# Performance work log

Measured on AMD Instinct MI355X. Metric: run time of the kernel, lower is better.

Reference implementation:

```python
import jax, jax.numpy as jnp
import numpy as np

B, N, D, H, S = 4, 32768, 256, 8, 64
DH = D // H  # 32


def setup_inputs() -> dict:
    key = jax.random.key(0)
    ks = jax.random.split(key, 8)
    s = 0.02
    return {
        "x": jax.random.normal(ks[0], (B, N, D), jnp.float32),
        "W_fx": jax.random.normal(ks[1], (D, D), jnp.float32) * s,
        "b_fx": jnp.zeros((D,), jnp.float32),
        "W_x": jax.random.normal(ks[2], (D, D), jnp.float32) * s,
        "b_x": jnp.zeros((D,), jnp.float32),
        "W_slice": jax.random.normal(ks[3], (DH, S), jnp.float32) * s,
        "b_slice": jnp.zeros((S,), jnp.float32),
        "temperature": jnp.full((1, H, 1, 1), 0.5, jnp.float32),
        "W_qkv": jax.random.normal(ks[4], (DH, 3 * DH), jnp.float32) * s,  # qkv_bias=False
        "W_out": jax.random.normal(ks[5], (D, D), jnp.float32) * s,
        "b_out": jnp.zeros((D,), jnp.float32),
    }


def reference(x, W_fx, b_fx, W_x, b_x, W_slice, b_slice, temperature, W_qkv, W_out, b_out):
    b, n, d = x.shape
    h, dh = H, d // H
    scale = dh ** -0.5
    # per-head projections: [b, h, n, dh]
    fx_mid = (x @ W_fx + b_fx).reshape(b, n, h, dh).transpose(0, 2, 1, 3)
    x_mid = (x @ W_x + b_x).reshape(b, n, h, dh).transpose(0, 2, 1, 3)
    # soft slice assignment: softmax over slices [b, h, n, s]
    logits = (x_mid @ W_slice + b_slice) / temperature
    slice_weights = jax.nn.softmax(logits, axis=-1)
    slice_norm = slice_weights.sum(axis=2)  # [b, h, s]
    # weighted pooling of points into slice tokens [b, h, s, dh]
    slice_token = jnp.einsum('bhnc,bhns->bhsc', fx_mid, slice_weights)
    slice_token = slice_token / (slice_norm[..., None] + 1e-5)
    # tiny attention among slice tokens
    q, k, v = jnp.split(slice_token @ W_qkv, 3, axis=-1)
    dots = jnp.einsum('bhsc,bhtc->bhst', q, k) * scale
    attn = jax.nn.softmax(dots, axis=-1)
    out_slice_token = attn @ v  # [b, h, s, dh]
    # scatter back to points [b, h, n, dh]
    out_x = jnp.einsum('bhsc,bhns->bhnc', out_slice_token, slice_weights)
    out_x = out_x.transpose(0, 2, 1, 3).reshape(b, n, d)
    return out_x @ W_out + b_out
```

## Files before the change

kernel.cpp:

```cpp
#include <hip/hip_runtime.h>
#include <math.h>

#define TS_N 32768
#define TS_M 131072

typedef short bf16x8 __attribute__((ext_vector_type(8)));
typedef float f32x4  __attribute__((ext_vector_type(4)));
typedef unsigned short us4 __attribute__((ext_vector_type(4)));
typedef unsigned short us8 __attribute__((ext_vector_type(8)));

static __device__ __forceinline__ unsigned short f2bf(float f) {
    unsigned u = __float_as_uint(f);
    u = u + 0x7FFF + ((u >> 16) & 1);
    return (unsigned short)(u >> 16);
}
static __device__ __forceinline__ float bf2f(unsigned short b) {
    return __uint_as_float(((unsigned)b) << 16);
}

__global__ __launch_bounds__(256) void k0_split(
    const float* __restrict__ src, unsigned short* __restrict__ h,
    unsigned short* __restrict__ l, int n4)
{
    for (int i = blockIdx.x * 256 + threadIdx.x; i < n4; i += gridDim.x * 256) {
        float4 v = ((const float4*)src)[i];
        us4 vh, vl;
        float c[4] = {v.x, v.y, v.z, v.w};
#pragma unroll
        for (int j = 0; j < 4; ++j) {
            unsigned short hh = f2bf(c[j]);
            vh[j] = hh;
            vl[j] = f2bf(c[j] - bf2f(hh));
        }
        ((us4*)h)[i] = vh;
        ((us4*)l)[i] = vl;
    }
}

__global__ __launch_bounds__(256) void k0_wt(
    const float* __restrict__ Wfx, const float* __restrict__ Wx,
    unsigned short* __restrict__ Wth, unsigned short* __restrict__ Wtl)
{
    const int n = blockIdx.x;
    const int wsel = blockIdx.y;
    const int k = threadIdx.x;
    const float v = (wsel ? Wx : Wfx)[k * 256 + n];
    const unsigned short hh = f2bf(v);
    const int idx = (wsel * 256 + n) * 256 + k;
    Wth[idx] = hh;
    Wtl[idx] = f2bf(v - bf2f(hh));
}

__global__ __launch_bounds__(256) void gemm_hl(
    const unsigned short* __restrict__ Ah, const unsigned short* __restrict__ Al,
    const unsigned short* __restrict__ Bth, const unsigned short* __restrict__ Btl,
    const float* __restrict__ bias, float* __restrict__ OUT,
    int K, long bsel)
{
    __shared__ unsigned short Alds[2][128 * 32];
    __shared__ unsigned short Blds[2][128 * 32];
    const int t = threadIdx.x;
    const int row0 = blockIdx.x * 128;
    const int n0 = blockIdx.y * 128;
    const long boff = (long)(row0 >> 15) * bsel;
    const unsigned short* Bhp = Bth + boff;
    const unsigned short* Blp = Btl + boff;

    const int w = t >> 6, l = t & 63;
    const int wm = w >> 1, wn = w & 1;
    const int lr = l & 15, lk = l >> 4;

    f32x4 acc[4][4];
#pragma unroll
    for (int i = 0; i < 4; ++i)
#pragma unroll
        for (int j = 0; j < 4; ++j) {
            acc[i][j][0] = 0.f; acc[i][j][1] = 0.f;
            acc[i][j][2] = 0.f; acc[i][j][3] = 0.f;
        }

    for (int kk = 0; kk < K; kk += 32) {
        bf16x8 stg[8];
#pragma unroll
        for (int g2i = 0; g2i < 2; ++g2i) {
            const int g2 = w + g2i * 4;
            const size_t ar = (size_t)(row0 + g2 * 16 + lr) * K + kk + lk * 8;
            const size_t br = (size_t)(n0 + g2 * 16 + lr) * K + kk + lk * 8;
            stg[g2i * 4 + 0] = *(const bf16x8*)&Ah[ar];
            stg[g2i * 4 + 1] = *(const bf16x8*)&Al[ar];
            stg[g2i * 4 + 2] = *(const bf16x8*)&Bhp[br];
            stg[g2i * 4 + 3] = *(const bf16x8*)&Blp[br];
        }
        __syncthreads();
#pragma unroll
        for (int g2i = 0; g2i < 2; ++g2i) {
            const int g2 = w + g2i * 4;
            const int lc = (g2 * 64 + l) * 8;
            *(bf16x8*)&Alds[0][lc] = stg[g2i * 4 + 0];
            *(bf16x8*)&Alds[1][lc] = stg[g2i * 4 + 1];
            *(bf16x8*)&Blds[0][lc] = stg[g2i * 4 + 2];
            *(bf16x8*)&Blds[1][lc] = stg[g2i * 4 + 3];
        }
        __syncthreads();

        bf16x8 ah[4], al[4], bh[4], bl[4];
#pragma unroll
        for (int g = 0; g < 4; ++g) {
            const int ac = (((wm * 4 + g) * 4 + lk) * 16 + lr) * 8;
            ah[g] = *(const bf16x8*)&Alds[0][ac];
            al[g] = *(const bf16x8*)&Alds[1][ac];
            const int bc = (((wn * 4 + g) * 4 + lk) * 16 + lr) * 8;
            bh[g] = *(const bf16x8*)&Blds[0][bc];
            bl[g] = *(const bf16x8*)&Blds[1][bc];
        }
#pragma unroll
        for (int m = 0; m < 4; ++m)
#pragma unroll
            for (int n = 0; n < 4; ++n) {
                acc[m][n] = __builtin_amdgcn_mfma_f32_16x16x32_bf16(ah[m], bh[n], acc[m][n], 0, 0, 0);
                acc[m][n] = __builtin_amdgcn_mfma_f32_16x16x32_bf16(ah[m], bl[n], acc[m][n], 0, 0, 0);
                acc[m][n] = __builtin_amdgcn_mfma_f32_16x16x32_bf16(al[m], bh[n], acc[m][n], 0, 0, 0);
            }
    }

    float bv[4];
#pragma unroll
    for (int n = 0; n < 4; ++n) bv[n] = bias[n0 + wn * 64 + n * 16 + lr];
#pragma unroll
    for (int m = 0; m < 4; ++m)
#pragma unroll
        for (int n = 0; n < 4; ++n) {
            const int col = n0 + wn * 64 + n * 16 + lr;
#pragma unroll
            for (int r = 0; r < 4; ++r) {
                const int row = row0 + wm * 64 + m * 16 + lk * 4 + r;
                OUT[(size_t)row * 256 + col] = acc[m][n][r] + bv[n];
            }
        }
}

__global__ __launch_bounds__(256) void k1b_slice_softmax(
    const float* __restrict__ XM, const float* __restrict__ Wsl,
    const float* __restrict__ bsl, const float* __restrict__ temp,
    unsigned short* __restrict__ SWh, unsigned short* __restrict__ SWl)
{
    __shared__ float XMs[32][68];
    __shared__ float Ws[32][68];
    __shared__ float Ls[64][68];
    const int t  = threadIdx.x;
    const int r0 = blockIdx.x * 64;
    const int h  = blockIdx.y;

    {
        const int m = t >> 2, cq = (t & 3) * 8;
        float4 v0 = *(const float4*)&XM[(size_t)(r0 + m) * 256 + h * 32 + cq];
        float4 v1 = *(const float4*)&XM[(size_t)(r0 + m) * 256 + h * 32 + cq + 4];
        XMs[cq + 0][m] = v0.x; XMs[cq + 1][m] = v0.y; XMs[cq + 2][m] = v0.z; XMs[cq + 3][m] = v0.w;
        XMs[cq + 4][m] = v1.x; XMs[cq + 5][m] = v1.y; XMs[cq + 6][m] = v1.z; XMs[cq + 7][m] = v1.w;
        const int wk = t >> 3, wn = (t & 7) * 8;
        float4 u0 = *(const float4*)&Wsl[wk * 64 + wn];
        float4 u1 = *(const float4*)&Wsl[wk * 64 + wn + 4];
        *(float4*)&Ws[wk][wn]     = u0;
        *(float4*)&Ws[wk][wn + 4] = u1;
    }
    __syncthreads();

    const int tx = t & 15, ty = t >> 4;
    float acc[4][4];
#pragma unroll
    for (int i = 0; i < 4; ++i)
#pragma unroll
        for (int j = 0; j < 4; ++j) acc[i][j] = 0.f;
#pragma unroll
    for (int c = 0; c < 32; ++c) {
        float4 av = *(const float4*)&XMs[c][ty * 4];
        float4 bv = *(const float4*)&Ws[c][tx * 4];
        float a_[4] = {av.x, av.y, av.z, av.w};
        float b_[4] = {bv.x, bv.y, bv.z, bv.w};
#pragma unroll
        for (int i = 0; i < 4; ++i)
#pragma unroll
            for (int j = 0; j < 4; ++j)
                acc[i][j] = fmaf(a_[i], b_[j], acc[i][j]);
    }
    const float invt = 1.0f / temp[h];
#pragma unroll
    for (int i = 0; i < 4; ++i)
#pragma unroll
        for (int j = 0; j < 4; ++j)
            Ls[ty * 4 + i][tx * 4 + j] = (acc[i][j] + bsl[tx * 4 + j]) * invt;
    __syncthreads();

    const int row = t >> 2, j4 = t & 3;
    float v[16];
    float mx = -1e30f;
#pragma unroll
    for (int i = 0; i < 16; ++i) { v[i] = Ls[row][j4 * 16 + i]; mx = fmaxf(mx, v[i]); }
    mx = fmaxf(mx, __shfl_xor(mx, 1));
    mx = fmaxf(mx, __shfl_xor(mx, 2));
    float sum = 0.f;
#pragma unroll
    for (int i = 0; i < 16; ++i) { v[i] = expf(v[i] - mx); sum += v[i]; }
    sum += __shfl_xor(sum, 1);
    sum += __shfl_xor(sum, 2);
    const float inv = 1.0f / sum;
#pragma unroll
    for (int q = 0; q < 4; ++q) {
        us4 oh, ol;
#pragma unroll
        for (int j = 0; j < 4; ++j) {
            const float o = v[q * 4 + j] * inv;
            const unsigned short hh = f2bf(o);
            oh[j] = hh;
            ol[j] = f2bf(o - bf2f(hh));
        }
        const size_t idx = (size_t)(r0 + row) * 512 + h * 64 + j4 * 16 + q * 4;
        *(us4*)&SWh[idx] = oh;
        *(us4*)&SWl[idx] = ol;
    }
}

__global__ __launch_bounds__(256) void k2_pool(
    const float* __restrict__ FX,
    const unsigned short* __restrict__ SWh, const unsigned short* __restrict__ SWl,
    float* __restrict__ PART, float* __restrict__ PARTN)
{
    __shared__ float SWs[2][64][68];
    __shared__ float FXs[2][64][36];
    const int t = threadIdx.x;
    const int chunk = blockIdx.x;
    const int bh = blockIdx.y;
    const int b = bh >> 3, h = bh & 7;
    const int gbase = b * TS_N + chunk * 512;

    const int rs = t >> 2;
    const int ch0 = t & 3;

    us8 swh[2], swl[2];
    float4 fxr[2];

    {
        const size_t swbase = (size_t)(gbase + rs) * 512 + h * 64;
        swh[0] = *(const us8*)&SWh[swbase + ch0 * 8];
        swh[1] = *(const us8*)&SWh[swbase + (ch0 + 4) * 8];
        swl[0] = *(const us8*)&SWl[swbase + ch0 * 8];
        swl[1] = *(const us8*)&SWl[swbase + (ch0 + 4) * 8];
        const size_t fxbase = (size_t)(gbase + rs) * 256 + h * 32;
        fxr[0] = *(const float4*)&FX[fxbase + ch0 * 4];
        fxr[1] = *(const float4*)&FX[fxbase + (ch0 + 4) * 4];
    }

    const int c = t & 31, sb = (t >> 5) * 8;
    float acc[8];
#pragma unroll
    for (int j = 0; j < 8; ++j) acc[j] = 0.f;
    float accn = 0.f;
    int buf = 0;

    for (int s = 0; s < 8; ++s) {
#pragma unroll
        for (int q = 0; q < 2; ++q) {
            const int cq = (ch0 + q * 4) * 8;
#pragma unroll
            for (int j = 0; j < 8; ++j)
                SWs[buf][rs][cq + j] = bf2f(swh[q][j]) + bf2f(swl[q][j]);
            *(float4*)&FXs[buf][rs][(ch0 + q * 4) * 4] = fxr[q];
        }
        __syncthreads();
        if (s < 7) {
            const int g2 = gbase + (s + 1) * 64 + rs;
            const size_t swbase = (size_t)g2 * 512 + h * 64;
            swh[0] = *(const us8*)&SWh[swbase + ch0 * 8];
            swh[1] = *(const us8*)&SWh[swbase + (ch0 + 4) * 8];
            swl[0] = *(const us8*)&SWl[swbase + ch0 * 8];
            swl[1] = *(const us8*)&SWl[swbase + (ch0 + 4) * 8];
            const size_t fxbase = (size_t)g2 * 256 + h * 32;
            fxr[0] = *(const float4*)&FX[fxbase + ch0 * 4];
            fxr[1] = *(const float4*)&FX[fxbase + (ch0 + 4) * 4];
        }
#pragma unroll 8
        for (int rr = 0; rr < 64; ++rr) {
            const float f = FXs[buf][rr][c];
            float4 s0 = *(const float4*)&SWs[buf][rr][sb];
            float4 s1 = *(const float4*)&SWs[buf][rr][sb + 4];
            acc[0] = fmaf(f, s0.x, acc[0]); acc[1] = fmaf(f, s0.y, acc[1]);
            acc[2] = fmaf(f, s0.z, acc[2]); acc[3] = fmaf(f, s0.w, acc[3]);
            acc[4] = fmaf(f, s1.x, acc[4]); acc[5] = fmaf(f, s1.y, acc[5]);
            acc[6] = fmaf(f, s1.z, acc[6]); acc[7] = fmaf(f, s1.w, acc[7]);
        }
        if (t < 64) {
#pragma unroll 8
            for (int rr = 0; rr < 64; ++rr) accn += SWs[buf][rr][t];
        }
        buf ^= 1;
    }

    const int pbase = (bh * 64 + chunk) * 2048;
#pragma unroll
    for (int j = 0; j < 8; ++j) PART[pbase + (sb + j) * 32 + c] = acc[j];
    if (t < 64) PARTN[(bh * 64 + chunk) * 64 + t] = accn;
}

__global__ __launch_bounds__(256) void k2b_reduce(
    const float* __restrict__ PART, const float* __restrict__ PARTN,
    float* __restrict__ ST, float* __restrict__ NORM)
{
    const int g = blockIdx.x, bh = blockIdx.y, t = threadIdx.x;
    const int e = g * 256 + t;
    float s = 0.f;
    for (int ch = 0; ch < 64; ++ch) s += PART[(size_t)(bh * 64 + ch) * 2048 + e];
    ST[bh * 2048 + e] = s;
    if (g == 0 && t < 64) {
        float sn = 0.f;
        for (int ch = 0; ch < 64; ++ch) sn += PARTN[(bh * 64 + ch) * 64 + t];
        NORM[bh * 64 + t] = sn;
    }
}

__global__ __launch_bounds__(64) void k3_attn(
    const float* __restrict__ ST, const float* __restrict__ NORM,
    const float* __restrict__ Wqkv, float* __restrict__ OST)
{
    __shared__ float Wq[32 * 96];
    __shared__ float Kl[64][32];
    __shared__ float Vl[64][32];
    __shared__ float Dl[64][68];
    const int bh = blockIdx.x;
    const int s  = threadIdx.x;

    for (int i = 0; i < 48; ++i) Wq[i * 64 + s] = Wqkv[i * 64 + s];
    float st[32];
    const float nrm = NORM[bh * 64 + s] + 1e-5f;
#pragma unroll
    for (int c = 0; c < 32; ++c) st[c] = ST[bh * 2048 + s * 32 + c] / nrm;
    __syncthreads();

    float q[32];
#pragma unroll
    for (int o4 = 0; o4 < 8; ++o4) {
        float ax = 0.f, ay = 0.f, az = 0.f, aw = 0.f;
#pragma unroll
        for (int c = 0; c < 32; ++c) {
            float4 w = *(const float4*)&Wq[c * 96 + o4 * 4];
            ax = fmaf(st[c], w.x, ax); ay = fmaf(st[c], w.y, ay);
            az = fmaf(st[c], w.z, az); aw = fmaf(st[c], w.w, aw);
        }
        q[o4 * 4 + 0] = ax; q[o4 * 4 + 1] = ay; q[o4 * 4 + 2] = az; q[o4 * 4 + 3] = aw;
    }
#pragma unroll
    for (int o4 = 0; o4 < 8; ++o4) {
        float ax = 0.f, ay = 0.f, az = 0.f, aw = 0.f;
#pragma unroll
        for (int c = 0; c < 32; ++c) {
            float4 w = *(const float4*)&Wq[c * 96 + 32 + o4 * 4];
            ax = fmaf(st[c], w.x, ax); ay = fmaf(st[c], w.y, ay);
            az = fmaf(st[c], w.z, az); aw = fmaf(st[c], w.w, aw);
        }
        float4 kv; kv.x = ax; kv.y = ay; kv.z = az; kv.w = aw;
        *(float4*)&Kl[s][o4 * 4] = kv;
    }
#pragma unroll
    for (int o4 = 0; o4 < 8; ++o4) {
        float ax = 0.f, ay = 0.f, az = 0.f, aw = 0.f;
#pragma unroll
        for (int c = 0; c < 32; ++c) {
            float4 w = *(const float4*)&Wq[c * 96 + 64 + o4 * 4];
            ax = fmaf(st[c], w.x, ax); ay = fmaf(st[c], w.y, ay);
            az = fmaf(st[c], w.z, az); aw = fmaf(st[c], w.w, aw);
        }
        float4 vv; vv.x = ax; vv.y = ay; vv.z = az; vv.w = aw;
        *(float4*)&Vl[s][o4 * 4] = vv;
    }
    __syncthreads();

    const float scale = 0.17677669529663687f;
    float mx = -1e30f;
    for (int t2 = 0; t2 < 64; ++t2) {
        float d = 0.f;
#pragma unroll
        for (int c4 = 0; c4 < 8; ++c4) {
            float4 kv = *(const float4*)&Kl[t2][c4 * 4];
            d = fmaf(q[c4 * 4 + 0], kv.x, d); d = fmaf(q[c4 * 4 + 1], kv.y, d);
            d = fmaf(q[c4 * 4 + 2], kv.z, d); d = fmaf(q[c4 * 4 + 3], kv.w, d);
        }
        d *= scale;
        Dl[s][t2] = d;
        mx = fmaxf(mx, d);
    }
    float sum = 0.f;
    for (int t2 = 0; t2 < 64; ++t2) { float e = expf(Dl[s][t2] - mx); Dl[s][t2] = e; sum += e; }
    const float inv = 1.0f / sum;
    float out[32];
#pragma unroll
    for (int c = 0; c < 32; ++c) out[c] = 0.f;
    for (int t2 = 0; t2 < 64; ++t2) {
        const float p = Dl[s][t2] * inv;
#pragma unroll
        for (int c4 = 0; c4 < 8; ++c4) {
            float4 vv = *(const float4*)&Vl[t2][c4 * 4];
            out[c4 * 4 + 0] = fmaf(p, vv.x, out[c4 * 4 + 0]);
            out[c4 * 4 + 1] = fmaf(p, vv.y, out[c4 * 4 + 1]);
            out[c4 * 4 + 2] = fmaf(p, vv.z, out[c4 * 4 + 2]);
            out[c4 * 4 + 3] = fmaf(p, vv.w, out[c4 * 4 + 3]);
        }
    }
#pragma unroll
    for (int c4 = 0; c4 < 8; ++c4) {
        float4 ov;
        ov.x = out[c4 * 4 + 0]; ov.y = out[c4 * 4 + 1];
        ov.z = out[c4 * 4 + 2]; ov.w = out[c4 * 4 + 3];
        *(float4*)&OST[bh * 2048 + s * 32 + c4 * 4] = ov;
    }
}

__global__ __launch_bounds__(256) void k3b_precomb(
    const float* __restrict__ OST, const float* __restrict__ Wout,
    unsigned short* __restrict__ Gth, unsigned short* __restrict__ Gtl)
{
    __shared__ float OSTs[64][36];
    __shared__ float Wc[32][256];
    const int bh = blockIdx.x;
    const int b = bh >> 3, h = bh & 7;
    const int t = threadIdx.x;

#pragma unroll
    for (int j = 0; j < 2; ++j) {
        const int e = (j * 256 + t) * 4;
        float4 v = *(const float4*)&OST[bh * 2048 + e];
        const int s = e >> 5, c = e & 31;
        OSTs[s][c + 0] = v.x; OSTs[s][c + 1] = v.y;
        OSTs[s][c + 2] = v.z; OSTs[s][c + 3] = v.w;
    }
#pragma unroll
    for (int j = 0; j < 8; ++j) {
        const int e = (j * 256 + t) * 4;
        const int c = e >> 8, o = e & 255;
        *(float4*)&Wc[c][o] = *(const float4*)&Wout[(h * 32 + c) * 256 + o];
    }
    __syncthreads();

    float wcol[32];
#pragma unroll
    for (int c = 0; c < 32; ++c) wcol[c] = Wc[c][t];

    for (int s = 0; s < 64; ++s) {
        float a = 0.f;
#pragma unroll
        for (int c = 0; c < 32; ++c) a = fmaf(OSTs[s][c], wcol[c], a);
        const unsigned short gh = f2bf(a);
        const size_t idx = ((size_t)(b * 256 + t)) * 512 + h * 64 + s;
        Gth[idx] = gh;
        Gtl[idx] = f2bf(a - bf2f(gh));
    }
}

extern "C" void kernel_launch(void* const* d_in, const int* in_sizes, int n_in,
                              void* d_out, int out_size, void* d_ws, size_t ws_size,
                              hipStream_t stream) {
    (void)in_sizes; (void)n_in; (void)out_size; (void)ws_size;
    const float* x    = (const float*)d_in[0];
    const float* Wfx  = (const float*)d_in[1];
    const float* bfx  = (const float*)d_in[2];
    const float* Wx   = (const float*)d_in[3];
    const float* bx   = (const float*)d_in[4];
    const float* Wsl  = (const float*)d_in[5];
    const float* bsl  = (const float*)d_in[6];
    const float* temp = (const float*)d_in[7];
    const float* Wqkv = (const float*)d_in[8];
    const float* Wout = (const float*)d_in[9];
    const float* bout = (const float*)d_in[10];
    float* out = (float*)d_out;
    char* w = (char*)d_ws;

    float* XM = (float*)w;
    char* sh = w + 134217728;
    unsigned short* Xh  = (unsigned short*)sh;
    unsigned short* Xl  = Xh + 33554432;
    unsigned short* SWh = (unsigned short*)sh;
    unsigned short* SWl = SWh + 67108864;
    char* p = w + 134217728 + 268435456;
    p += 8388608;
    p += 262144;
    float* ST    = (float*)p;            p += 262144;
    float* NORM  = (float*)p;            p += 8192;
    float* OST   = (float*)p;            p += 262144;
    unsigned short* Gth = (unsigned short*)p; p += 1048576;
    unsigned short* Gtl = (unsigned short*)p; p += 1048576;
    unsigned short* Wth = (unsigned short*)p; p += 262144;
    unsigned short* Wtl = (unsigned short*)p; p += 262144;
    float* PART  = XM;
    float* PARTN = XM + 4194304;
    float* FX = out;

    k0_split<<<2048, 256, 0, stream>>>(x, Xh, Xl, TS_M * 256 / 4);
    k0_wt<<<dim3(256, 2), 256, 0, stream>>>(Wfx, Wx, Wth, Wtl);
    gemm_hl<<<dim3(TS_M / 128, 2), 256, 0, stream>>>(Xh, Xl, Wth, Wtl, bfx, FX, 256, 0);
    gemm_hl<<<dim3(TS_M / 128, 2), 256, 0, stream>>>(Xh, Xl, Wth + 65536, Wtl + 65536, bx, XM, 256, 0);
    k1b_slice_softmax<<<dim3(TS_M / 64, 8), 256, 0, stream>>>(XM, Wsl, bsl, temp, SWh, SWl);
    k2_pool<<<dim3(64, 32), 256, 0, stream>>>(FX, SWh, SWl, PART, PARTN);
    k2b_reduce<<<dim3(8, 32), 256, 0, stream>>>(PART, PARTN, ST, NORM);
    k3_attn<<<32, 64, 0, stream>>>(ST, NORM, Wqkv, OST);
    k3b_precomb<<<32, 256, 0, stream>>>(OST, Wout, Gth, Gtl);
    gemm_hl<<<dim3(TS_M / 128, 2), 256, 0, stream>>>(SWh, SWl, Gth, Gtl, bout, out, 512, 131072);
}
```

Before: 695.1 us.

## Fuse projection GEMMs, prefetch next K tile into registers, XCD-aware block mapping

The two input-projection GEMMs (W_fx and W_x) become a single launch. Block indices are remapped so that the column tiles sharing one row block sit on the same XCD, which improves L2 reuse of the A operand. The GEMM body now prefetches the next K-slice from global memory into registers while the MFMAs of the current slice run, with K as a template parameter so the loop is fully known at compile time. Register pressure rises from holding the prefetch buffer, and the mapping assumes round-robin dispatch of blocks across 8 XCDs.

New measurement: 668.7 us. -3.8%, faster.

```diff
diff --git a/kernel.cpp b/kernel.cpp
--- a/kernel.cpp
+++ b/kernel.cpp
@@ -51,21 +51,16 @@
     Wtl[idx] = f2bf(v - bf2f(hh));
 }
 
-__global__ __launch_bounds__(256) void gemm_hl(
+template<int K>
+static __device__ __forceinline__ void gemm_body(
     const unsigned short* __restrict__ Ah, const unsigned short* __restrict__ Al,
     const unsigned short* __restrict__ Bth, const unsigned short* __restrict__ Btl,
     const float* __restrict__ bias, float* __restrict__ OUT,
-    int K, long bsel)
+    int row0, int n0)
 {
     __shared__ unsigned short Alds[2][128 * 32];
     __shared__ unsigned short Blds[2][128 * 32];
     const int t = threadIdx.x;
-    const int row0 = blockIdx.x * 128;
-    const int n0 = blockIdx.y * 128;
-    const long boff = (long)(row0 >> 15) * bsel;
-    const unsigned short* Bhp = Bth + boff;
-    const unsigned short* Blp = Btl + boff;
-
     const int w = t >> 6, l = t & 63;
     const int wm = w >> 1, wn = w & 1;
     const int lr = l & 15, lk = l >> 4;
@@ -79,29 +74,43 @@
             acc[i][j][2] = 0.f; acc[i][j][3] = 0.f;
         }
 
-    for (int kk = 0; kk < K; kk += 32) {
-        bf16x8 stg[8];
+    bf16x8 sA[2][2], sB[2][2];
+#pragma unroll
+    for (int g2i = 0; g2i < 2; ++g2i) {
+        const int g2 = w + g2i * 4;
+        const size_t ar = (size_t)(row0 + g2 * 16 + lr) * K + lk * 8;
+        const size_t br = (size_t)(g2 * 16 + lr) * K + lk * 8;
+        sA[g2i][0] = *(const bf16x8*)&Ah[ar];
+        sA[g2i][1] = *(const bf16x8*)&Al[ar];
+        sB[g2i][0] = *(const bf16x8*)&Bth[br];
+        sB[g2i][1] = *(const bf16x8*)&Btl[br];
+    }
+
+    const int NSTEP = K / 32;
+    for (int step = 0; step < NSTEP; ++step) {
+        __syncthreads();
 #pragma unroll
         for (int g2i = 0; g2i < 2; ++g2i) {
-            const int g2 = w + g2i * 4;
-            const size_t ar = (size_t)(row0 + g2 * 16 + lr) * K + kk + lk * 8;
-            const size_t br = (size_t)(n0 + g2 * 16 + lr) * K + kk + lk * 8;
-            stg[g2i * 4 + 0] = *(const bf16x8*)&Ah[ar];
-            stg[g2i * 4 + 1] = *(const bf16x8*)&Al[ar];
-            stg[g2i * 4 + 2] = *(const bf16x8*)&Bhp[br];
-            stg[g2i * 4 + 3] = *(const bf16x8*)&Blp[br];
+            const int lc = ((w + g2i * 4) * 64 + l) * 8;
+            *(bf16x8*)&Alds[0][lc] = sA[g2i][0];
+            *(bf16x8*)&Alds[1][lc] = sA[g2i][1];
+            *(bf16x8*)&Blds[0][lc] = sB[g2i][0];
+            *(bf16x8*)&Blds[1][lc] = sB[g2i][1];
         }
         __syncthreads();
-#pragma unroll
-        for (int g2i = 0; g2i < 2; ++g2i) {
-            const int g2 = w + g2i * 4;
-            const int lc = (g2 * 64 + l) * 8;
-            *(bf16x8*)&Alds[0][lc] = stg[g2i * 4 + 0];
-            *(bf16x8*)&Alds[1][lc] = stg[g2i * 4 + 1];
-            *(bf16x8*)&Blds[0][lc] = stg[g2i * 4 + 2];
-            *(bf16x8*)&Blds[1][lc] = stg[g2i * 4 + 3];
-        }
-        __syncthreads();
+        if (step < NSTEP - 1) {
+            const int kk = (step + 1) * 32;
+#pragma unroll
+            for (int g2i = 0; g2i < 2; ++g2i) {
+                const int g2 = w + g2i * 4;
+                const size_t ar = (size_t)(row0 + g2 * 16 + lr) * K + kk + lk * 8;
+                const size_t br = (size_t)(g2 * 16 + lr) * K + kk + lk * 8;
+                sA[g2i][0] = *(const bf16x8*)&Ah[ar];
+                sA[g2i][1] = *(const bf16x8*)&Al[ar];
+                sB[g2i][0] = *(const bf16x8*)&Bth[br];
+                sB[g2i][1] = *(const bf16x8*)&Btl[br];
+            }
+        }
 
         bf16x8 ah[4], al[4], bh[4], bl[4];
 #pragma unroll
@@ -137,6 +146,40 @@
                 OUT[(size_t)row * 256 + col] = acc[m][n][r] + bv[n];
             }
         }
+}
+
+__global__ __launch_bounds__(256) void k1_gemm(
+    const unsigned short* __restrict__ Ah, const unsigned short* __restrict__ Al,
+    const unsigned short* __restrict__ Wth, const unsigned short* __restrict__ Wtl,
+    const float* __restrict__ bfx, const float* __restrict__ bx,
+    float* __restrict__ FX, float* __restrict__ XM)
+{
+    const int L = blockIdx.x;
+    const int xcd = L & 7, ii = L >> 3;
+    const int rb = xcd * 128 + (ii >> 2), nsel = ii & 3;
+    const int row0 = rb * 128;
+    const int n0 = (nsel & 1) * 128;
+    const unsigned short* Bth = Wth + (nsel >> 1) * 65536 + n0 * 256;
+    const unsigned short* Btl = Wtl + (nsel >> 1) * 65536 + n0 * 256;
+    const float* bias = (nsel >> 1) ? bx : bfx;
+    float* OUT = (nsel >> 1) ? XM : FX;
+    gemm_body<256>(Ah, Al, Bth, Btl, bias, OUT, row0, n0);
+}
+
+__global__ __launch_bounds__(256) void k4_gemm(
+    const unsigned short* __restrict__ SWh, const unsigned short* __restrict__ SWl,
+    const unsigned short* __restrict__ Gth, const unsigned short* __restrict__ Gtl,
+    const float* __restrict__ bout, float* __restrict__ out)
+{
+    const int L = blockIdx.x;
+    const int xcd = L & 7, ii = L >> 3;
+    const int rb = xcd * 128 + (ii >> 1), nsel = ii & 1;
+    const int row0 = rb * 128;
+    const int n0 = nsel * 128;
+    const int b = row0 >> 15;
+    const unsigned short* Bth = Gth + ((size_t)b * 256 + n0) * 512;
+    const unsigned short* Btl = Gtl + ((size_t)b * 256 + n0) * 512;
+    gemm_body<512>(SWh, SWl, Bth, Btl, bout, out, row0, n0);
 }
 
 __global__ __launch_bounds__(256) void k1b_slice_softmax(
@@ -494,12 +537,11 @@
 
     k0_split<<<2048, 256, 0, stream>>>(x, Xh, Xl, TS_M * 256 / 4);
     k0_wt<<<dim3(256, 2), 256, 0, stream>>>(Wfx, Wx, Wth, Wtl);
-    gemm_hl<<<dim3(TS_M / 128, 2), 256, 0, stream>>>(Xh, Xl, Wth, Wtl, bfx, FX, 256, 0);
-    gemm_hl<<<dim3(TS_M / 128, 2), 256, 0, stream>>>(Xh, Xl, Wth + 65536, Wtl + 65536, bx, XM, 256, 0);
+    k1_gemm<<<4096, 256, 0, stream>>>(Xh, Xl, Wth, Wtl, bfx, bx, FX, XM);
     k1b_slice_softmax<<<dim3(TS_M / 64, 8), 256, 0, stream>>>(XM, Wsl, bsl, temp, SWh, SWl);
     k2_pool<<<dim3(64, 32), 256, 0, stream>>>(FX, SWh, SWl, PART, PARTN);
     k2b_reduce<<<dim3(8, 32), 256, 0, stream>>>(PART, PARTN, ST, NORM);
     k3_attn<<<32, 64, 0, stream>>>(ST, NORM, Wqkv, OST);
     k3b_precomb<<<32, 256, 0, stream>>>(OST, Wout, Gth, Gtl);
-    gemm_hl<<<dim3(TS_M / 128, 2), 256, 0, stream>>>(SWh, SWl, Gth, Gtl, bout, out, 512, 131072);
-}
+    k4_gemm<<<2048, 256, 0, stream>>>(SWh, SWl, Gth, Gtl, bout, out);
+}
```
